# Kernel optimization log

Hardware: AMD Instinct MI355X
Metric: run time of the kernel (lower is better)

The kernel has to match this reference:

```python
import jax, jax.numpy as jnp
import numpy as np

# ---- static structure (from LastFMModel source) ----
COUNTS = (50000, 80000, 10000)   # user, item, tag node counts
FEAT, HID, INTRA, INTER = 256, 128, 64, 128
E = 500000                        # edges per metapath hop
# hops listed leaf->target as (src_type, dst_type, edge_type)
MP_USER = [[(0, 1, 0), (1, 0, 1)],
           [(0, 1, 0), (1, 2, 2), (2, 1, 3), (1, 0, 1)],
           [(0, 0, 4)]]
MP_ITEM = [[(1, 0, 1), (0, 1, 0)],
           [(1, 2, 2), (2, 1, 3)],
           [(1, 0, 1), (0, 0, 4), (0, 1, 0)]]
# get_gcn_encoder: etype in {1,2,4} -> encoder 1, {0,3} -> encoder 2
GCN_GROUP = {0: 2, 1: 1, 2: 1, 3: 2, 4: 1}
OFFSETS = (0, COUNTS[0], COUNTS[0] + COUNTS[1])


def _gen_edges(mps, rng):
    rows = []
    for hops in mps:
        for (st, dt, et) in hops:
            rows.append(np.stack([rng.integers(0, COUNTS[st], E),
                                  rng.integers(0, COUNTS[dt], E)]))
    return jnp.asarray(np.stack(rows), jnp.int32)


def setup_inputs() -> dict:
    rng = np.random.default_rng(0)
    ks = jax.random.split(jax.random.key(0), 16)
    n_total = sum(COUNTS)
    s = 0.05
    d = {}
    d['features'] = jax.random.normal(ks[0], (n_total, FEAT), jnp.float32)
    d['edges_user'] = _gen_edges(MP_USER, rng)
    d['edges_item'] = _gen_edges(MP_ITEM, rng)
    d['perm_user'] = jnp.asarray(rng.permutation(COUNTS[0]), jnp.int32)
    d['perm_item'] = jnp.asarray(rng.permutation(COUNTS[1]), jnp.int32)
    d['W_type'] = jax.random.normal(ks[1], (3, FEAT, HID), jnp.float32) * s
    d['b_type'] = jnp.zeros((3, HID), jnp.float32)
    d['comp_vec'] = jax.random.normal(ks[2], (5, HID), jnp.float32) * s
    d['W_gcn'] = jax.random.normal(ks[3], (3, HID, HID), jnp.float32) * s
    d['b_gcn'] = jnp.zeros((3, HID), jnp.float32)
    d['fc_u'] = jax.random.normal(ks[4], (3, HID, INTRA), jnp.float32) * s
    d['fcr_u'] = jax.random.normal(ks[5], (3, INTRA, HID), jnp.float32) * s
    d['V_u'] = jax.random.normal(ks[6], (3 * INTRA, INTER), jnp.float32) * s
    d['Vr_u'] = jax.random.normal(ks[7], (INTER, 3 * INTRA), jnp.float32) * s
    d['fc_i'] = jax.random.normal(ks[8], (3, HID, INTRA), jnp.float32) * s
    d['fcr_i'] = jax.random.normal(ks[9], (3, INTRA, HID), jnp.float32) * s
    d['V_i'] = jax.random.normal(ks[10], (3 * INTRA, INTER), jnp.float32) * s
    d['Vr_i'] = jax.random.normal(ks[11], (INTER, 3 * INTRA), jnp.float32) * s
    return d


def _propagate(h_src, src, dst, etype, n_dst, comp_vec, W_gcn, b_gcn):
    # CompGCN composition (elementwise) + GraphConv norm='right' (in-degree mean)
    msg = h_src[src] * comp_vec[etype]                                  # [E, HID]
    agg = jax.ops.segment_sum(msg, dst, num_segments=n_dst)
    deg = jax.ops.segment_sum(jnp.ones_like(dst, jnp.float32), dst, num_segments=n_dst)
    h = agg / jnp.clip(deg, 1.0)[:, None]
    g = GCN_GROUP[etype]
    return h @ W_gcn[g] + b_gcn[g]


def _fusion(outs, fc, fcr, V, Vr):
    # AutoMvFusion: per-view intra projection, shared inter fusion,
    # reconstruction loss + pairwise view orthogonality loss
    z_list = [jnp.tanh(h @ fc[p]) for p, h in enumerate(outs)]          # [N, INTRA] each
    z = jnp.concatenate(z_list, axis=1)                                 # [N, 3*INTRA]
    fused = z @ V                                                       # [N, INTER]
    z_rec = fused @ Vr
    re = jnp.float32(0.0)
    for p, h in enumerate(outs):
        h_rec = z_rec[:, p * INTRA:(p + 1) * INTRA] @ fcr[p]
        re = re + jnp.mean((h_rec - h) ** 2)
    orth = jnp.float32(0.0)
    for p in range(3):
        for q in range(p + 1, 3):
            g = z_list[p].T @ z_list[q]                                 # [INTRA, INTRA]
            orth = orth + jnp.mean(g ** 2)
    return fused, re + orth


def _run_layer(mp_hops, edges, perm, t_feats, comp_vec, W_gcn, b_gcn, fc, fcr, V, Vr):
    k = 0
    outs = []
    for hops in mp_hops:
        h = t_feats[hops[0][0]]           # leaf-type transformed features
        for (st, dt, et) in hops:
            h = _propagate(h, edges[k, 0], edges[k, 1], et, COUNTS[dt],
                           comp_vec, W_gcn, b_gcn)
            k += 1
        outs.append(h[perm])              # new_index_arrangement reindex
    return _fusion(outs, fc, fcr, V, Vr)


def reference(features, edges_user, edges_item, perm_user, perm_item,
              W_type, b_type, comp_vec, W_gcn, b_gcn,
              fc_u, fcr_u, V_u, Vr_u, fc_i, fcr_i, V_i, Vr_i):
    # NodeTransform: per-type linear + activation (dropout off at eval)
    t_feats = [jax.nn.relu(features[OFFSETS[t]:OFFSETS[t] + COUNTS[t]] @ W_type[t] + b_type[t])
               for t in range(3)]
    h_user, loss_u = _run_layer(MP_USER, edges_user, perm_user, t_feats,
                                comp_vec, W_gcn, b_gcn, fc_u, fcr_u, V_u, Vr_u)
    h_item, loss_i = _run_layer(MP_ITEM, edges_item, perm_item, t_feats,
                                comp_vec, W_gcn, b_gcn, fc_i, fcr_i, V_i, Vr_i)
    return h_user, h_item, loss_u + loss_i
```

## Files before the change

### kernel.cpp

```cpp
#include <hip/hip_runtime.h>

typedef unsigned short u16;
typedef unsigned int   u32;

#define ACT_NONE 0
#define ACT_RELU 1
#define ACT_TANH 2

#define E_EDGES 500000
#define RP_STRIDE 80004
#define NCH 62
#define CH 8192
#define HSTRIDE 19456

using s8vec = __attribute__((ext_vector_type(8))) short;
using f4vec = __attribute__((ext_vector_type(4))) float;

__device__ __forceinline__ float bf2f(u16 u) {
  union { u32 b; float f; } v; v.b = ((u32)u) << 16; return v.f;
}
__device__ __forceinline__ u16 f2bf(float x) {
  union { float f; u32 b; } v; v.f = x;
  u32 r = v.b + 0x7fffu + ((v.b >> 16) & 1u);
  return (u16)(r >> 16);
}
__device__ __forceinline__ void acc8(float* acc, uint4 v) {
  union { u32 b; float f; } cv;
  cv.b = v.x << 16;         acc[0] += cv.f;
  cv.b = v.x & 0xffff0000u; acc[1] += cv.f;
  cv.b = v.y << 16;         acc[2] += cv.f;
  cv.b = v.y & 0xffff0000u; acc[3] += cv.f;
  cv.b = v.z << 16;         acc[4] += cv.f;
  cv.b = v.z & 0xffff0000u; acc[5] += cv.f;
  cv.b = v.w << 16;         acc[6] += cv.f;
  cv.b = v.w & 0xffff0000u; acc[7] += cv.f;
}

struct TJob { const float* src; u16* dst; const float* scale; int R; int C; };
struct TBatch { TJob j[24]; };
__global__ __launch_bounds__(256) void transpose_b_k(TBatch b) {
  TJob jb = b.j[blockIdx.y];
  int i = blockIdx.x * 256 + threadIdx.x;
  if (i >= jb.R * jb.C) return;
  int r = i / jb.C, c = i % jb.C;
  float v = jb.src[i];
  if (jb.scale) v *= jb.scale[r];
  jb.dst[(size_t)c * jb.R + r] = f2bf(v);
}

struct IBatch { const int* perm[2]; int* ip[2]; int n[2]; };
__global__ __launch_bounds__(256) void iperm_b_k(IBatch b) {
  int y = blockIdx.y;
  int i = blockIdx.x * 256 + threadIdx.x;
  if (i < b.n[y]) b.ip[y][b.perm[y][i]] = i;
}

struct CsrP { int n[14]; int sh[14]; int P[14]; };

__global__ __launch_bounds__(256) void csr_hist_k(
    const int* __restrict__ eu, const int* __restrict__ ei,
    int* __restrict__ hista, CsrP cp) {
  const int hop = blockIdx.y, chunk = blockIdx.x;
  const int P = cp.P[hop], sh = cp.sh[hop];
  __shared__ int hist[320];
  for (int i = threadIdx.x; i < P; i += 256) hist[i] = 0;
  __syncthreads();
  const int* edges = (hop < 7) ? eu : ei;
  const int h7 = (hop < 7) ? hop : hop - 7;
  const int* dstp = edges + (size_t)(h7 * 2 + 1) * E_EDGES;
  const int e0 = chunk * CH;
  const int e1 = min(E_EDGES, e0 + CH);
  for (int e = e0 + threadIdx.x * 4; e < e1; e += 1024) {
    int4 d4 = *(const int4*)(dstp + e);
    atomicAdd(&hist[d4.x >> sh], 1);
    atomicAdd(&hist[d4.y >> sh], 1);
    atomicAdd(&hist[d4.z >> sh], 1);
    atomicAdd(&hist[d4.w >> sh], 1);
  }
  __syncthreads();
  for (int i = threadIdx.x; i < P; i += 256)
    hista[(size_t)hop * HSTRIDE + i * NCH + chunk] = hist[i];
}

__global__ __launch_bounds__(256) void csr_scan_k(int* __restrict__ hista, CsrP cp) {
  const int hop = blockIdx.x;
  const int L = cp.P[hop] * NCH;
  int* a = hista + (size_t)hop * HSTRIDE;
  const int per = (L + 255) >> 8;
  const int lo = threadIdx.x * per;
  const int hi = min(L, lo + per);
  int s = 0;
  for (int i = lo; i < hi; ++i) s += a[i];
  __shared__ int lds[256];
  lds[threadIdx.x] = s;
  __syncthreads();
  for (int off = 1; off < 256; off <<= 1) {
    int v = (threadIdx.x >= off) ? lds[threadIdx.x - off] : 0;
    __syncthreads();
    lds[threadIdx.x] += v;
    __syncthreads();
  }
  int run = threadIdx.x ? lds[threadIdx.x - 1] : 0;
  for (int i = lo; i < hi; ++i) { int v = a[i]; a[i] = run; run += v; }
}

__global__ __launch_bounds__(256) void csr_scatter_k(
    const int* __restrict__ eu, const int* __restrict__ ei,
    const int* __restrict__ hista, u32* __restrict__ bp, CsrP cp) {
  const int hop = blockIdx.y, chunk = blockIdx.x;
  const int P = cp.P[hop], sh = cp.sh[hop];
  const u32 fm = (1u << sh) - 1u;
  __shared__ int cur[320];
  for (int i = threadIdx.x; i < P; i += 256)
    cur[i] = hista[(size_t)hop * HSTRIDE + i * NCH + chunk];
  __syncthreads();
  const int* edges = (hop < 7) ? eu : ei;
  const int h7 = (hop < 7) ? hop : hop - 7;
  const int* srcp = edges + (size_t)(h7 * 2) * E_EDGES;
  const int* dstp = srcp + E_EDGES;
  u32* b = bp + (size_t)hop * E_EDGES;
  const int e0 = chunk * CH;
  const int e1 = min(E_EDGES, e0 + CH);
  for (int e = e0 + threadIdx.x * 4; e < e1; e += 1024) {
    int4 d4 = *(const int4*)(dstp + e);
    int4 s4 = *(const int4*)(srcp + e);
    int dd[4] = {d4.x, d4.y, d4.z, d4.w};
    int ss[4] = {s4.x, s4.y, s4.z, s4.w};
#pragma unroll
    for (int j = 0; j < 4; ++j) {
      int pos = atomicAdd(&cur[dd[j] >> sh], 1);
      b[pos] = (u32)ss[j] | (((u32)dd[j] & fm) << 24);
    }
  }
}

__global__ __launch_bounds__(256) void csr_fine_k(
    const u32* __restrict__ bp, const int* __restrict__ hista,
    int* __restrict__ rowptrb, int* __restrict__ esrcb, CsrP cp) {
  const int hop = blockIdx.y, p = blockIdx.x;
  const int P = cp.P[hop];
  if (p >= P) return;
  const int n = cp.n[hop], sh = cp.sh[hop], W = 1 << sh;
  const int* fl = hista + (size_t)hop * HSTRIDE;
  const int beg = fl[p * NCH];
  const int end = (p + 1 < P) ? fl[(p + 1) * NCH] : E_EDGES;
  const int nb = min(W, n - p * W);
  const int tid = threadIdx.x;

  __shared__ int fh[256];
  __shared__ int sc[256];
  __shared__ int cur[256];
  fh[tid] = 0;
  __syncthreads();
  const u32* b = bp + (size_t)hop * E_EDGES;
  for (int i = beg + tid; i < end; i += 256)
    atomicAdd(&fh[b[i] >> 24], 1);
  __syncthreads();
  sc[tid] = fh[tid];
  __syncthreads();
  for (int off = 1; off < 256; off <<= 1) {
    int v = (tid >= off) ? sc[tid - off] : 0;
    __syncthreads();
    sc[tid] += v;
    __syncthreads();
  }
  const int excl = tid ? sc[tid - 1] : 0;
  int* rowptr = rowptrb + (size_t)hop * RP_STRIDE;
  if (tid < nb) rowptr[p * W + tid] = beg + excl;
  cur[tid] = beg + excl;
  if (p == P - 1 && tid == 0) rowptr[n] = E_EDGES;
  __syncthreads();
  int* esrc = esrcb + (size_t)hop * E_EDGES;
  for (int i = beg + tid; i < end; i += 256) {
    u32 v = b[i];
    int pos = atomicAdd(&cur[v >> 24], 1);
    esrc[pos] = (int)(v & 0xFFFFFFu);
  }
}

struct HopJob {
  const u16* h; const int* rowptr; const int* esrc;
  const u16* Bt; const float* bias; u16* out;
  const int* iperm; int n; int permout;
};
struct HopBatch { HopJob j[6]; };

__global__ __launch_bounds__(256) void hop_b_k(HopBatch batch) {
  const HopJob jb = batch.j[blockIdx.y];
  const int rbase = blockIdx.x * 64;
  if (rbase >= jb.n) return;

  __shared__ u16 bts[128 * 128];
  const int tid = threadIdx.x;
  for (int i = tid; i < 128 * 16; i += 256) {
    int nn = i >> 4, g = i & 15;
    int gs = (g & 8) | ((g ^ nn) & 7);
    *(uint4*)(&bts[nn * 128 + gs * 8]) = *(const uint4*)(jb.Bt + (size_t)nn * 128 + g * 8);
  }
  __syncthreads();

  const int wave = tid >> 6;
  const int lane = tid & 63;
  const int kgrp = lane >> 4;
  const int lid  = lane & 15;
  const int d = rbase + wave * 16 + lid;

  float a0[8] = {0,0,0,0,0,0,0,0}, a1[8] = {0,0,0,0,0,0,0,0};
  float a2[8] = {0,0,0,0,0,0,0,0}, a3[8] = {0,0,0,0,0,0,0,0};
  int s0 = 0, s1 = 0;
  if (d < jb.n) { s0 = jb.rowptr[d]; s1 = jb.rowptr[d + 1]; }
  const u16* hk = jb.h + kgrp * 8;
  int i = s0;
  for (; i + 1 < s1; i += 2) {
    const u16* ra = hk + (size_t)jb.esrc[i] * 128;
    const u16* rb = hk + (size_t)jb.esrc[i + 1] * 128;
    uint4 va0 = *(const uint4*)(ra);      uint4 vb0 = *(const uint4*)(rb);
    uint4 va1 = *(const uint4*)(ra + 32); uint4 vb1 = *(const uint4*)(rb + 32);
    uint4 va2 = *(const uint4*)(ra + 64); uint4 vb2 = *(const uint4*)(rb + 64);
    uint4 va3 = *(const uint4*)(ra + 96); uint4 vb3 = *(const uint4*)(rb + 96);
    acc8(a0, va0); acc8(a1, va1); acc8(a2, va2); acc8(a3, va3);
    acc8(a0, vb0); acc8(a1, vb1); acc8(a2, vb2); acc8(a3, vb3);
  }
  if (i < s1) {
    const u16* ra = hk + (size_t)jb.esrc[i] * 128;
    acc8(a0, *(const uint4*)(ra));
    acc8(a1, *(const uint4*)(ra + 32));
    acc8(a2, *(const uint4*)(ra + 64));
    acc8(a3, *(const uint4*)(ra + 96));
  }
  const float rs = 1.0f / fmaxf((float)(s1 - s0), 1.0f);
  s8vec f0, f1, f2, f3;
#pragma unroll
  for (int j = 0; j < 8; ++j) f0[j] = (short)f2bf(a0[j] * rs);
#pragma unroll
  for (int j = 0; j < 8; ++j) f1[j] = (short)f2bf(a1[j] * rs);
#pragma unroll
  for (int j = 0; j < 8; ++j) f2[j] = (short)f2bf(a2[j] * rs);
#pragma unroll
  for (int j = 0; j < 8; ++j) f3[j] = (short)f2bf(a3[j] * rs);

#pragma unroll
  for (int t = 0; t < 8; ++t) {
    f4vec c = {0.f, 0.f, 0.f, 0.f};
    const int bn = t * 16 + lid;
    int g = kgrp;
    int gs = (g & 8) | ((g ^ bn) & 7);
    c = __builtin_amdgcn_mfma_f32_16x16x32_bf16(f0, *(const s8vec*)(&bts[bn * 128 + gs * 8]), c, 0, 0, 0);
    g = 4 + kgrp; gs = (g & 8) | ((g ^ bn) & 7);
    c = __builtin_amdgcn_mfma_f32_16x16x32_bf16(f1, *(const s8vec*)(&bts[bn * 128 + gs * 8]), c, 0, 0, 0);
    g = 8 + kgrp; gs = (g & 8) | ((g ^ bn) & 7);
    c = __builtin_amdgcn_mfma_f32_16x16x32_bf16(f2, *(const s8vec*)(&bts[bn * 128 + gs * 8]), c, 0, 0, 0);
    g = 12 + kgrp; gs = (g & 8) | ((g ^ bn) & 7);
    c = __builtin_amdgcn_mfma_f32_16x16x32_bf16(f3, *(const s8vec*)(&bts[bn * 128 + gs * 8]), c, 0, 0, 0);
    const int col = bn;
    const float bb = jb.bias[col];
#pragma unroll
    for (int j = 0; j < 4; ++j) {
      int r = rbase + wave * 16 + kgrp * 4 + j;
      if (r < jb.n) {
        float v = c[j] + bb;
        int ro = jb.permout ? jb.iperm[r] : r;
        jb.out[(size_t)ro * 128 + col] = f2bf(v);
      }
    }
  }
}

struct GemmJob {
  const void* A; const u16* Bt; const float* bias; void* C;
  const u16* target; float* loss; u16* Ct; int M;
};
struct GemmBatch { GemmJob j[3]; };

template <int K, int N, int ACT, int AMODE, bool CF32, bool SQDIFF, bool CTR>
__global__ __launch_bounds__(256) void gemm_b_k(
    GemmBatch batch, int ldA, int ldC, int ldCt) {
  static_assert(K % 32 == 0 && N % 16 == 0, "");
  const GemmJob jb = batch.j[blockIdx.y];
  const int rbase0 = blockIdx.x * 64;
  if (rbase0 >= jb.M) return;

  __shared__ u16 bts[N * K];
  __shared__ float red[4];

  const int tid = threadIdx.x;
  for (int i = tid; i < N * (K / 8); i += 256) {
    int n = i / (K / 8);
    int g = i % (K / 8);
    int gs = (g & ~7) | ((g ^ n) & 7);
    *(uint4*)(&bts[n * K + gs * 8]) = *(const uint4*)(jb.Bt + (size_t)n * K + g * 8);
  }
  __syncthreads();

  const int wave = tid >> 6;
  const int lane = tid & 63;
  const int kgrp = lane >> 4;
  const int rbase = rbase0 + wave * 16;
  const int rowA = rbase + (lane & 15);
  const bool av = rowA < jb.M;

  s8vec afr[K / 32];
  if constexpr (AMODE == 1) {
    const float* arow = (const float*)jb.A + (size_t)rowA * ldA;
#pragma unroll
    for (int kt = 0; kt < K / 32; ++kt) {
      s8vec fr = {0, 0, 0, 0, 0, 0, 0, 0};
      if (av) {
        const float* p = arow + kt * 32 + kgrp * 8;
        float4 fa = *(const float4*)(p);
        float4 fb = *(const float4*)(p + 4);
        fr[0] = (short)f2bf(fa.x); fr[1] = (short)f2bf(fa.y);
        fr[2] = (short)f2bf(fa.z); fr[3] = (short)f2bf(fa.w);
        fr[4] = (short)f2bf(fb.x); fr[5] = (short)f2bf(fb.y);
        fr[6] = (short)f2bf(fb.z); fr[7] = (short)f2bf(fb.w);
      }
      afr[kt] = fr;
    }
  } else {
    const u16* arow = (const u16*)jb.A + (size_t)rowA * ldA;
#pragma unroll
    for (int kt = 0; kt < K / 32; ++kt) {
      s8vec fr = {0, 0, 0, 0, 0, 0, 0, 0};
      if (av) fr = *(const s8vec*)(arow + kt * 32 + kgrp * 8);
      afr[kt] = fr;
    }
  }

  float sqsum = 0.0f;
#pragma unroll
  for (int t = 0; t < N / 16; ++t) {
    f4vec acc = {0.f, 0.f, 0.f, 0.f};
    const int bn = t * 16 + (lane & 15);
#pragma unroll
    for (int kt = 0; kt < K / 32; ++kt) {
      int g = kt * 4 + kgrp;
      int gs = (g & ~7) | ((g ^ bn) & 7);
      s8vec bfr = *(const s8vec*)(&bts[bn * K + gs * 8]);
      acc = __builtin_amdgcn_mfma_f32_16x16x32_bf16(afr[kt], bfr, acc, 0, 0, 0);
    }
    const int col = t * 16 + (lane & 15);
    float bb = jb.bias ? jb.bias[col] : 0.0f;
#pragma unroll
    for (int j = 0; j < 4; ++j) {
      int r = rbase + kgrp * 4 + j;
      if (r < jb.M) {
        float v = acc[j] + bb;
        if constexpr (ACT == ACT_RELU) v = fmaxf(v, 0.0f);
        if constexpr (ACT == ACT_TANH) v = tanhf(v);
        if constexpr (SQDIFF) {
          float dd = v - bf2f(jb.target[(size_t)r * N + col]);
          sqsum += dd * dd;
        } else if constexpr (CF32) {
          ((float*)jb.C)[(size_t)r * ldC + col] = v;
        } else {
          ((u16*)jb.C)[(size_t)r * ldC + col] = f2bf(v);
        }
        if constexpr (CTR) {
          jb.Ct[(size_t)col * ldCt + r] = f2bf(v);
        }
      }
    }
  }

  if constexpr (SQDIFF) {
#pragma unroll
    for (int off = 32; off > 0; off >>= 1) sqsum += __shfl_down(sqsum, off);
    if (lane == 0) red[wave] = sqsum;
    __syncthreads();
    if (tid == 0) atomicAdd(jb.loss, red[0] + red[1] + red[2] + red[3]);
  }
}

#define GRAM_NKB 40
__global__ __launch_bounds__(256) void gram_k(
    const u16* __restrict__ zt, int NP, float* __restrict__ G3) {
  const int pair = blockIdx.y;
  const int p = (pair == 2) ? 1 : 0;
  const int q = (pair == 0) ? 1 : 2;
  const int wave = threadIdx.x >> 6;
  const int lane = threadIdx.x & 63;
  const int kgrp = lane >> 4, lid = lane & 15;

  const int KC = (((NP + GRAM_NKB - 1) / GRAM_NKB) + 31) & ~31;
  const int kbeg = blockIdx.x * KC;
  const int kend = min(NP, kbeg + KC);

  const u16* arow = zt + (size_t)(p * 64 + wave * 16 + lid) * NP;
  const u16* brow0 = zt + (size_t)(q * 64 + 0 * 16 + lid) * NP;
  const u16* brow1 = zt + (size_t)(q * 64 + 1 * 16 + lid) * NP;
  const u16* brow2 = zt + (size_t)(q * 64 + 2 * 16 + lid) * NP;
  const u16* brow3 = zt + (size_t)(q * 64 + 3 * 16 + lid) * NP;

  f4vec acc0 = {0.f, 0.f, 0.f, 0.f};
  f4vec acc1 = {0.f, 0.f, 0.f, 0.f};
  f4vec acc2 = {0.f, 0.f, 0.f, 0.f};
  f4vec acc3 = {0.f, 0.f, 0.f, 0.f};

  for (int k0 = kbeg; k0 < kend; k0 += 32) {
    const int ko = k0 + kgrp * 8;
    s8vec af = *(const s8vec*)(arow + ko);
    s8vec b0 = *(const s8vec*)(brow0 + ko);
    s8vec b1 = *(const s8vec*)(brow1 + ko);
    s8vec b2 = *(const s8vec*)(brow2 + ko);
    s8vec b3 = *(const s8vec*)(brow3 + ko);
    acc0 = __builtin_amdgcn_mfma_f32_16x16x32_bf16(af, b0, acc0, 0, 0, 0);
    acc1 = __builtin_amdgcn_mfma_f32_16x16x32_bf16(af, b1, acc1, 0, 0, 0);
    acc2 = __builtin_amdgcn_mfma_f32_16x16x32_bf16(af, b2, acc2, 0, 0, 0);
    acc3 = __builtin_amdgcn_mfma_f32_16x16x32_bf16(af, b3, acc3, 0, 0, 0);
  }

  float* g = G3 + (size_t)pair * 4096;
  const int mrow = wave * 16 + kgrp * 4;
#pragma unroll
  for (int j = 0; j < 4; ++j) {
    atomicAdd(&g[(mrow + j) * 64 + 0 * 16 + lid], acc0[j]);
    atomicAdd(&g[(mrow + j) * 64 + 1 * 16 + lid], acc1[j]);
    atomicAdd(&g[(mrow + j) * 64 + 2 * 16 + lid], acc2[j]);
    atomicAdd(&g[(mrow + j) * 64 + 3 * 16 + lid], acc3[j]);
  }
}

__global__ __launch_bounds__(256) void loss_k(
    const float* __restrict__ G, const float* __restrict__ RE,
    float* __restrict__ out) {
  float s = 0.f;
  for (int i = threadIdx.x; i < 2 * 3 * 4096; i += 256) { float g = G[i]; s += g * g; }
#pragma unroll
  for (int off = 32; off > 0; off >>= 1) s += __shfl_down(s, off);
  __shared__ float red[4];
  int wave = threadIdx.x >> 6, lane = threadIdx.x & 63;
  if (lane == 0) red[wave] = s;
  __syncthreads();
  if (threadIdx.x == 0) {
    float orth = (red[0] + red[1] + red[2] + red[3]) / 4096.0f;
    float loss = orth + RE[0] / (50000.0f * 128.0f) + RE[1] / (80000.0f * 128.0f);
    out[0] = loss;
  }
}

static const int COUNTS_H[3] = {50000, 80000, 10000};
static const int OFFS_H[3]   = {0, 50000, 130000};
static const int GRP_H[5]    = {2, 1, 1, 2, 1};
static const int HOPN[14] = {80000, 50000, 80000, 10000, 80000, 50000, 50000,
                             50000, 80000, 10000, 80000, 50000, 50000, 80000};

extern "C" void kernel_launch(void* const* d_in, const int* in_sizes, int n_in,
                              void* d_out, int out_size, void* d_ws, size_t ws_size,
                              hipStream_t stream) {
  (void)in_sizes; (void)n_in; (void)out_size; (void)ws_size;

  const float* features = (const float*)d_in[0];
  const int* e_user   = (const int*)d_in[1];
  const int* e_item   = (const int*)d_in[2];
  const int* perm_u   = (const int*)d_in[3];
  const int* perm_i   = (const int*)d_in[4];
  const float* W_type = (const float*)d_in[5];
  const float* b_type = (const float*)d_in[6];
  const float* comp   = (const float*)d_in[7];
  const float* W_gcn  = (const float*)d_in[8];
  const float* b_gcn  = (const float*)d_in[9];
  const float* fc[2]  = {(const float*)d_in[10], (const float*)d_in[14]};
  const float* fcr[2] = {(const float*)d_in[11], (const float*)d_in[15]};
  const float* V[2]   = {(const float*)d_in[12], (const float*)d_in[16]};
  const float* Vr[2]  = {(const float*)d_in[13], (const float*)d_in[17]};
  float* out = (float*)d_out;

  char* base = (char*)d_ws;
  size_t off = 0;
  auto alloc = [&](size_t b) -> void* {
    void* p = base + off;
    off = (off + b + 255) & ~(size_t)255;
    return p;
  };
  u16* TF    = (u16*)alloc(140000ull * 128 * 2);
  u16* HB    = (u16*)alloc(330000ull * 128 * 2);
  u16* OUTSu = (u16*)alloc(3ull * 50000 * 128 * 2);
  u16* OUTSi = (u16*)alloc(3ull * 80000 * 128 * 2);
  int* HISTA    = (int*)alloc(14ull * HSTRIDE * 4);
  int* ROWPTR14 = (int*)alloc(14ull * RP_STRIDE * 4);
  int* ESRC14   = (int*)alloc(14ull * E_EDGES * 4);
  int* IPERM    = (int*)alloc(130000ull * 4);
  u16* WT_TYPE = (u16*)alloc(3ull * 128 * 256 * 2);
  u16* BT_HOP  = (u16*)alloc(5ull * 128 * 128 * 2);
  u16* FCT     = (u16*)alloc(6ull * 64 * 128 * 2);
  u16* VT      = (u16*)alloc(2ull * 128 * 192 * 2);
  u16* VRT     = (u16*)alloc(2ull * 192 * 128 * 2);
  u16* FCRT    = (u16*)alloc(6ull * 128 * 64 * 2);
  float* G   = (float*)alloc((2 * 3 * 4096 + 2) * 4);
  float* RE  = G + 2 * 3 * 4096;

  u32* BP   = (u32*)HB;
  u16* Z    = HB;
  u16* ZREC = HB + 80000ull * 192;
  u16* ZT   = (u16*)HISTA;

  const int hbrow[7] = {0, 80000, 160000, 170000, 220000, 230000, 280000};
  auto HBp = [&](int c) { return HB + (size_t)hbrow[c] * 128; };
  auto RP  = [&](int g) { return ROWPTR14 + (size_t)g * RP_STRIDE; };
  auto ES  = [&](int g) { return ESRC14 + (size_t)g * E_EDGES; };
  auto BT  = [&](int et) { return BT_HOP + (size_t)et * 128 * 128; };
  auto BG  = [&](int et) { return b_gcn + (size_t)GRP_H[et] * 128; };

  TBatch tb;
  int tj = 0;
  for (int t = 0; t < 3; ++t)
    tb.j[tj++] = {W_type + (size_t)t * 256 * 128, WT_TYPE + (size_t)t * 128 * 256, nullptr, 256, 128};
  for (int et = 0; et < 5; ++et)
    tb.j[tj++] = {W_gcn + (size_t)GRP_H[et] * 128 * 128, BT_HOP + (size_t)et * 128 * 128,
                  comp + (size_t)et * 128, 128, 128};
  for (int L = 0; L < 2; ++L)
    for (int p = 0; p < 3; ++p)
      tb.j[tj++] = {fc[L] + (size_t)p * 128 * 64, FCT + (size_t)(L * 3 + p) * 64 * 128, nullptr, 128, 64};
  for (int L = 0; L < 2; ++L)
    for (int p = 0; p < 3; ++p)
      tb.j[tj++] = {fcr[L] + (size_t)p * 64 * 128, FCRT + (size_t)(L * 3 + p) * 128 * 64, nullptr, 64, 128};
  for (int L = 0; L < 2; ++L)
    tb.j[tj++] = {V[L], VT + (size_t)L * 128 * 192, nullptr, 192, 128};
  for (int L = 0; L < 2; ++L)
    tb.j[tj++] = {Vr[L], VRT + (size_t)L * 192 * 128, nullptr, 128, 192};
  transpose_b_k<<<dim3(128, 24), 256, 0, stream>>>(tb);

  IBatch ib;
  ib.perm[0] = perm_u; ib.ip[0] = IPERM;          ib.n[0] = 50000;
  ib.perm[1] = perm_i; ib.ip[1] = IPERM + 50000;  ib.n[1] = 80000;
  iperm_b_k<<<dim3(313, 2), 256, 0, stream>>>(ib);

  CsrP cpp;
  for (int g = 0; g < 14; ++g) {
    cpp.n[g] = HOPN[g];
    cpp.sh[g] = (HOPN[g] <= 10000) ? 6 : 8;
    cpp.P[g] = (HOPN[g] + (1 << cpp.sh[g]) - 1) >> cpp.sh[g];
  }
  csr_hist_k<<<dim3(NCH, 14), 256, 0, stream>>>(e_user, e_item, HISTA, cpp);
  csr_scan_k<<<dim3(14), 256, 0, stream>>>(HISTA, cpp);
  csr_scatter_k<<<dim3(NCH, 14), 256, 0, stream>>>(e_user, e_item, HISTA, BP, cpp);
  csr_fine_k<<<dim3(313, 14), 256, 0, stream>>>(BP, HISTA, ROWPTR14, ESRC14, cpp);
  hipMemsetAsync(G, 0, (2 * 3 * 4096 + 2) * 4, stream);

  {
    GemmBatch nb;
    for (int t = 0; t < 3; ++t)
      nb.j[t] = {features + (size_t)OFFS_H[t] * 256, WT_TYPE + (size_t)t * 128 * 256,
                 b_type + (size_t)t * 128, TF + (size_t)OFFS_H[t] * 128,
                 nullptr, nullptr, nullptr, COUNTS_H[t]};
    gemm_b_k<256, 128, ACT_RELU, 1, false, false, false>
        <<<dim3(1250, 3), 256, 0, stream>>>(nb, 256, 128, 0);
  }

  const u16* TF0 = TF;
  const u16* TF1 = TF + 50000ull * 128;
  const int* IPu = IPERM;
  const int* IPi = IPERM + 50000;

  HopBatch L0, L1, L2, L3;
  L0.j[0] = {TF0, RP(0),  ES(0),  BT(0), BG(0), HBp(0), nullptr, 80000, 0};
  L0.j[1] = {TF0, RP(2),  ES(2),  BT(0), BG(0), HBp(1), nullptr, 80000, 0};
  L0.j[2] = {TF0, RP(6),  ES(6),  BT(4), BG(4), OUTSu + 2ull * 50000 * 128, IPu, 50000, 1};
  L0.j[3] = {TF1, RP(7),  ES(7),  BT(1), BG(1), HBp(3), nullptr, 50000, 0};
  L0.j[4] = {TF1, RP(9),  ES(9),  BT(2), BG(2), HBp(4), nullptr, 10000, 0};
  L0.j[5] = {TF1, RP(11), ES(11), BT(1), BG(1), HBp(5), nullptr, 50000, 0};
  L1.j[0] = {HBp(0), RP(1),  ES(1),  BT(1), BG(1), OUTSu, IPu, 50000, 1};
  L1.j[1] = {HBp(1), RP(3),  ES(3),  BT(2), BG(2), HBp(2), nullptr, 10000, 0};
  L1.j[2] = {HBp(3), RP(8),  ES(8),  BT(0), BG(0), OUTSi, IPi, 80000, 1};
  L1.j[3] = {HBp(4), RP(10), ES(10), BT(3), BG(3), OUTSi + 1ull * 80000 * 128, IPi, 80000, 1};
  L1.j[4] = {HBp(5), RP(12), ES(12), BT(4), BG(4), HBp(6), nullptr, 50000, 0};
  L1.j[5] = L1.j[4];
  L2.j[0] = {HBp(2), RP(4),  ES(4),  BT(3), BG(3), HBp(0), nullptr, 80000, 0};
  L2.j[1] = {HBp(6), RP(13), ES(13), BT(0), BG(0), OUTSi + 2ull * 80000 * 128, IPi, 80000, 1};
  L2.j[2] = L2.j[1]; L2.j[3] = L2.j[1]; L2.j[4] = L2.j[1]; L2.j[5] = L2.j[1];
  L3.j[0] = {HBp(0), RP(5), ES(5), BT(1), BG(1), OUTSu + 1ull * 50000 * 128, IPu, 50000, 1};
  L3.j[1] = L3.j[0]; L3.j[2] = L3.j[0]; L3.j[3] = L3.j[0]; L3.j[4] = L3.j[0]; L3.j[5] = L3.j[0];

  hop_b_k<<<dim3(1250, 6), 256, 0, stream>>>(L0);
  hop_b_k<<<dim3(1250, 5), 256, 0, stream>>>(L1);
  hop_b_k<<<dim3(1250, 2), 256, 0, stream>>>(L2);
  hop_b_k<<<dim3(782, 1), 256, 0, stream>>>(L3);

  for (int L = 0; L < 2; ++L) {
    const int nL = L ? 80000 : 50000;
    const int NP = (nL + 31) & ~31;
    u16* OUTS_L = L ? OUTSi : OUTSu;
    const size_t pstride = (size_t)nL * 128;
    const dim3 gg((unsigned)((nL + 63) / 64));

    if (NP != nL)
      hipMemsetAsync(ZT, 0, (size_t)192 * NP * 2, stream);

    GemmBatch fb;
    for (int p = 0; p < 3; ++p)
      fb.j[p] = {OUTS_L + p * pstride, FCT + (size_t)(L * 3 + p) * 64 * 128, nullptr,
                 Z + p * 64, nullptr, nullptr, ZT + (size_t)p * 64 * NP, nL};
    gemm_b_k<128, 64, ACT_TANH, 0, false, false, true>
        <<<dim3(gg.x, 3), 256, 0, stream>>>(fb, 128, 192, NP);

    gram_k<<<dim3(GRAM_NKB, 3), 256, 0, stream>>>(ZT, NP, G + (size_t)L * 3 * 4096);

    float* fused = out + (L ? 6400000 : 0);
    GemmBatch vb;
    vb.j[0] = {Z, VT + (size_t)L * 128 * 192, nullptr, fused, nullptr, nullptr, nullptr, nL};
    vb.j[1] = vb.j[0]; vb.j[2] = vb.j[0];
    gemm_b_k<192, 128, ACT_NONE, 0, true, false, false>
        <<<dim3(gg.x, 1), 256, 0, stream>>>(vb, 192, 128, 0);

    GemmBatch rb;
    rb.j[0] = {fused, VRT + (size_t)L * 192 * 128, nullptr, ZREC, nullptr, nullptr, nullptr, nL};
    rb.j[1] = rb.j[0]; rb.j[2] = rb.j[0];
    gemm_b_k<128, 192, ACT_NONE, 1, false, false, false>
        <<<dim3(gg.x, 1), 256, 0, stream>>>(rb, 128, 192, 0);

    GemmBatch sb;
    for (int p = 0; p < 3; ++p)
      sb.j[p] = {ZREC + p * 64, FCRT + (size_t)(L * 3 + p) * 128 * 64, nullptr,
                 nullptr, OUTS_L + p * pstride, RE + L, nullptr, nL};
    gemm_b_k<64, 128, ACT_NONE, 0, false, true, false>
        <<<dim3(gg.x, 3), 256, 0, stream>>>(sb, 192, 0, 0);
  }

  loss_k<<<1, 256, 0, stream>>>(G, RE, out + 16640000);
}
```

Before: 1.109 ms.

## Fuse fusion-stage V, Vr and reconstruction-loss GEMMs into one kernel, batch both layers

Three GEMM launches per layer (V projection, Vr reconstruction, per-path fcr reconstruction with squared-difference loss) become one vfuse_k kernel. It keeps the fused tile and reconstructed Z in shared memory instead of writing ZREC to global and reading it back. The user and item layers are also batched into single launches for the tanh GEMM and the Gram kernel, giving separate Z/ZT buffers per layer. B operands in the fused kernel are read straight from global memory rather than staged in LDS, which may add load traffic in exchange for less intermediate round-tripping.

```diff
diff --git a/kernel.cpp b/kernel.cpp
--- a/kernel.cpp
+++ b/kernel.cpp
@@ -239,6 +239,13 @@
 #pragma unroll
   for (int j = 0; j < 8; ++j) f3[j] = (short)f2bf(a3[j] * rs);
 
+  int rout[4];
+#pragma unroll
+  for (int j = 0; j < 4; ++j) {
+    int rv = rbase + wave * 16 + kgrp * 4 + j;
+    rout[j] = (rv < jb.n) ? (jb.permout ? jb.iperm[rv] : rv) : -1;
+  }
+
 #pragma unroll
   for (int t = 0; t < 8; ++t) {
     f4vec c = {0.f, 0.f, 0.f, 0.f};
@@ -252,15 +259,12 @@
     c = __builtin_amdgcn_mfma_f32_16x16x32_bf16(f2, *(const s8vec*)(&bts[bn * 128 + gs * 8]), c, 0, 0, 0);
     g = 12 + kgrp; gs = (g & 8) | ((g ^ bn) & 7);
     c = __builtin_amdgcn_mfma_f32_16x16x32_bf16(f3, *(const s8vec*)(&bts[bn * 128 + gs * 8]), c, 0, 0, 0);
-    const int col = bn;
-    const float bb = jb.bias[col];
+    const float bb = jb.bias[bn];
 #pragma unroll
     for (int j = 0; j < 4; ++j) {
-      int r = rbase + wave * 16 + kgrp * 4 + j;
-      if (r < jb.n) {
+      if (rout[j] >= 0) {
         float v = c[j] + bb;
-        int ro = jb.permout ? jb.iperm[r] : r;
-        jb.out[(size_t)ro * 128 + col] = f2bf(v);
+        jb.out[(size_t)rout[j] * 128 + bn] = f2bf(v);
       }
     }
   }
@@ -268,20 +272,19 @@
 
 struct GemmJob {
   const void* A; const u16* Bt; const float* bias; void* C;
-  const u16* target; float* loss; u16* Ct; int M;
+  u16* Ct; int M; int ldCt;
 };
-struct GemmBatch { GemmJob j[3]; };
-
-template <int K, int N, int ACT, int AMODE, bool CF32, bool SQDIFF, bool CTR>
+struct GemmBatch { GemmJob j[6]; };
+
+template <int K, int N, int ACT, int AMODE, bool CF32, bool CTR>
 __global__ __launch_bounds__(256) void gemm_b_k(
-    GemmBatch batch, int ldA, int ldC, int ldCt) {
+    GemmBatch batch, int ldA, int ldC) {
   static_assert(K % 32 == 0 && N % 16 == 0, "");
   const GemmJob jb = batch.j[blockIdx.y];
   const int rbase0 = blockIdx.x * 64;
   if (rbase0 >= jb.M) return;
 
   __shared__ u16 bts[N * K];
-  __shared__ float red[4];
 
   const int tid = threadIdx.x;
   for (int i = tid; i < N * (K / 8); i += 256) {
@@ -326,7 +329,6 @@
     }
   }
 
-  float sqsum = 0.0f;
 #pragma unroll
   for (int t = 0; t < N / 16; ++t) {
     f4vec acc = {0.f, 0.f, 0.f, 0.f};
@@ -347,34 +349,150 @@
         float v = acc[j] + bb;
         if constexpr (ACT == ACT_RELU) v = fmaxf(v, 0.0f);
         if constexpr (ACT == ACT_TANH) v = tanhf(v);
-        if constexpr (SQDIFF) {
-          float dd = v - bf2f(jb.target[(size_t)r * N + col]);
-          sqsum += dd * dd;
-        } else if constexpr (CF32) {
+        if constexpr (CF32) {
           ((float*)jb.C)[(size_t)r * ldC + col] = v;
         } else {
           ((u16*)jb.C)[(size_t)r * ldC + col] = f2bf(v);
         }
         if constexpr (CTR) {
-          jb.Ct[(size_t)col * ldCt + r] = f2bf(v);
+          jb.Ct[(size_t)col * jb.ldCt + r] = f2bf(v);
         }
       }
     }
   }
-
-  if constexpr (SQDIFF) {
-#pragma unroll
-    for (int off = 32; off > 0; off >>= 1) sqsum += __shfl_down(sqsum, off);
-    if (lane == 0) red[wave] = sqsum;
-    __syncthreads();
-    if (tid == 0) atomicAdd(jb.loss, red[0] + red[1] + red[2] + red[3]);
-  }
+}
+
+struct VFJob {
+  const u16* Z;
+  const u16* VT;
+  const u16* VRT;
+  const u16* FCRT;
+  const u16* target;
+  float* fused;
+  float* loss;
+  int M;
+};
+
+__global__ __launch_bounds__(256) void vfuse_k(VFJob j0, VFJob j1) {
+  const VFJob jb = blockIdx.y ? j1 : j0;
+  const int rbase = blockIdx.x * 64;
+  if (rbase >= jb.M) return;
+
+  __shared__ u16 ftile[64 * 128];
+  __shared__ u16 ztile[64 * 192];
+  __shared__ float red[4];
+
+  const int tid = threadIdx.x;
+  const int wave = tid >> 6;
+  const int lane = tid & 63;
+  const int kgrp = lane >> 4;
+  const int lid  = lane & 15;
+  const int arow_l = wave * 16 + lid;
+  const int rowA = rbase + arow_l;
+  const bool av = rowA < jb.M;
+
+  s8vec az[6];
+#pragma unroll
+  for (int kt = 0; kt < 6; ++kt) {
+    s8vec fr = {0, 0, 0, 0, 0, 0, 0, 0};
+    if (av) fr = *(const s8vec*)(jb.Z + (size_t)rowA * 192 + kt * 32 + kgrp * 8);
+    az[kt] = fr;
+  }
+#pragma unroll
+  for (int t = 0; t < 8; ++t) {
+    f4vec acc = {0.f, 0.f, 0.f, 0.f};
+    const int bn = t * 16 + lid;
+    const u16* brow = jb.VT + (size_t)bn * 192;
+#pragma unroll
+    for (int kt = 0; kt < 6; ++kt)
+      acc = __builtin_amdgcn_mfma_f32_16x16x32_bf16(az[kt], *(const s8vec*)(brow + kt * 32 + kgrp * 8), acc, 0, 0, 0);
+    const int g = bn >> 3;
+#pragma unroll
+    for (int j = 0; j < 4; ++j) {
+      int rl = wave * 16 + kgrp * 4 + j;
+      int r = rbase + rl;
+      float v = acc[j];
+      int gs = (g & 8) | ((g ^ rl) & 7);
+      if (r < jb.M) {
+        jb.fused[(size_t)r * 128 + bn] = v;
+        ftile[rl * 128 + gs * 8 + (bn & 7)] = f2bf(v);
+      } else {
+        ftile[rl * 128 + gs * 8 + (bn & 7)] = 0;
+      }
+    }
+  }
+  __syncthreads();
+
+  s8vec af[4];
+#pragma unroll
+  for (int kt = 0; kt < 4; ++kt) {
+    int ga = kt * 4 + kgrp;
+    int gs = (ga & 8) | ((ga ^ arow_l) & 7);
+    af[kt] = *(const s8vec*)(&ftile[arow_l * 128 + gs * 8]);
+  }
+#pragma unroll
+  for (int t = 0; t < 12; ++t) {
+    f4vec acc = {0.f, 0.f, 0.f, 0.f};
+    const int bn = t * 16 + lid;
+    const u16* brow = jb.VRT + (size_t)bn * 128;
+#pragma unroll
+    for (int kt = 0; kt < 4; ++kt)
+      acc = __builtin_amdgcn_mfma_f32_16x16x32_bf16(af[kt], *(const s8vec*)(brow + kt * 32 + kgrp * 8), acc, 0, 0, 0);
+    const int g = bn >> 3;
+#pragma unroll
+    for (int j = 0; j < 4; ++j) {
+      int rl = wave * 16 + kgrp * 4 + j;
+      int gs = (g & ~7) | ((g ^ rl) & 7);
+      ztile[rl * 192 + gs * 8 + (bn & 7)] = f2bf(acc[j]);
+    }
+  }
+  __syncthreads();
+
+  float sqsum = 0.0f;
+#pragma unroll
+  for (int p = 0; p < 3; ++p) {
+    s8vec aq[2];
+#pragma unroll
+    for (int kt = 0; kt < 2; ++kt) {
+      int ga = p * 8 + kt * 4 + kgrp;
+      int gs = (ga & ~7) | ((ga ^ arow_l) & 7);
+      aq[kt] = *(const s8vec*)(&ztile[arow_l * 192 + gs * 8]);
+    }
+    const u16* fp = jb.FCRT + (size_t)p * 128 * 64;
+    const u16* tgt = jb.target + (size_t)p * jb.M * 128;
+#pragma unroll
+    for (int t = 0; t < 8; ++t) {
+      f4vec acc = {0.f, 0.f, 0.f, 0.f};
+      const int bn = t * 16 + lid;
+      const u16* brow = fp + (size_t)bn * 64;
+#pragma unroll
+      for (int kt = 0; kt < 2; ++kt)
+        acc = __builtin_amdgcn_mfma_f32_16x16x32_bf16(aq[kt], *(const s8vec*)(brow + kt * 32 + kgrp * 8), acc, 0, 0, 0);
+#pragma unroll
+      for (int j = 0; j < 4; ++j) {
+        int r = rbase + wave * 16 + kgrp * 4 + j;
+        if (r < jb.M) {
+          float dd = acc[j] - bf2f(tgt[(size_t)r * 128 + bn]);
+          sqsum += dd * dd;
+        }
+      }
+    }
+  }
+#pragma unroll
+  for (int off = 32; off > 0; off >>= 1) sqsum += __shfl_down(sqsum, off);
+  if (lane == 0) red[wave] = sqsum;
+  __syncthreads();
+  if (tid == 0) atomicAdd(jb.loss, red[0] + red[1] + red[2] + red[3]);
 }
 
 #define GRAM_NKB 40
 __global__ __launch_bounds__(256) void gram_k(
-    const u16* __restrict__ zt, int NP, float* __restrict__ G3) {
-  const int pair = blockIdx.y;
+    const u16* __restrict__ zt0, const u16* __restrict__ zt1,
+    int NP0, int NP1, float* __restrict__ G) {
+  const int layer = blockIdx.y / 3;
+  const int pair = blockIdx.y % 3;
+  const u16* zt = layer ? zt1 : zt0;
+  const int NP = layer ? NP1 : NP0;
   const int p = (pair == 2) ? 1 : 0;
   const int q = (pair == 0) ? 1 : 2;
   const int wave = threadIdx.x >> 6;
@@ -409,7 +527,7 @@
     acc3 = __builtin_amdgcn_mfma_f32_16x16x32_bf16(af, b3, acc3, 0, 0, 0);
   }
 
-  float* g = G3 + (size_t)pair * 4096;
+  float* g = G + (size_t)layer * 3 * 4096 + (size_t)pair * 4096;
   const int mrow = wave * 16 + kgrp * 4;
 #pragma unroll
   for (int j = 0; j < 4; ++j) {
@@ -490,9 +608,11 @@
   float* RE  = G + 2 * 3 * 4096;
 
   u32* BP   = (u32*)HB;
-  u16* Z    = HB;
-  u16* ZREC = HB + 80000ull * 192;
-  u16* ZT   = (u16*)HISTA;
+  u16* Z0   = HB;
+  u16* Z1   = HB + 9600000ull;
+  const int NP0 = 50016, NP1 = 80032;
+  u16* ZT0  = (u16*)HISTA;
+  u16* ZT1  = TF;
 
   const int hbrow[7] = {0, 80000, 160000, 170000, 220000, 230000, 280000};
   auto HBp = [&](int c) { return HB + (size_t)hbrow[c] * 128; };
@@ -538,13 +658,13 @@
   hipMemsetAsync(G, 0, (2 * 3 * 4096 + 2) * 4, stream);
 
   {
-    GemmBatch nb;
+    GemmBatch nb = {};
     for (int t = 0; t < 3; ++t)
       nb.j[t] = {features + (size_t)OFFS_H[t] * 256, WT_TYPE + (size_t)t * 128 * 256,
                  b_type + (size_t)t * 128, TF + (size_t)OFFS_H[t] * 128,
-                 nullptr, nullptr, nullptr, COUNTS_H[t]};
-    gemm_b_k<256, 128, ACT_RELU, 1, false, false, false>
-        <<<dim3(1250, 3), 256, 0, stream>>>(nb, 256, 128, 0);
+                 nullptr, COUNTS_H[t], 0};
+    gemm_b_k<256, 128, ACT_RELU, 1, false, false>
+        <<<dim3(1250, 3), 256, 0, stream>>>(nb, 256, 128);
   }
 
   const u16* TF0 = TF;
@@ -576,44 +696,28 @@
   hop_b_k<<<dim3(1250, 2), 256, 0, stream>>>(L2);
   hop_b_k<<<dim3(782, 1), 256, 0, stream>>>(L3);
 
-  for (int L = 0; L < 2; ++L) {
-    const int nL = L ? 80000 : 50000;
-    const int NP = (nL + 31) & ~31;
-    u16* OUTS_L = L ? OUTSi : OUTSu;
-    const size_t pstride = (size_t)nL * 128;
-    const dim3 gg((unsigned)((nL + 63) / 64));
-
-    if (NP != nL)
-      hipMemsetAsync(ZT, 0, (size_t)192 * NP * 2, stream);
-
-    GemmBatch fb;
-    for (int p = 0; p < 3; ++p)
-      fb.j[p] = {OUTS_L + p * pstride, FCT + (size_t)(L * 3 + p) * 64 * 128, nullptr,
-                 Z + p * 64, nullptr, nullptr, ZT + (size_t)p * 64 * NP, nL};
-    gemm_b_k<128, 64, ACT_TANH, 0, false, false, true>
-        <<<dim3(gg.x, 3), 256, 0, stream>>>(fb, 128, 192, NP);
-
-    gram_k<<<dim3(GRAM_NKB, 3), 256, 0, stream>>>(ZT, NP, G + (size_t)L * 3 * 4096);
-
-    float* fused = out + (L ? 6400000 : 0);
-    GemmBatch vb;
-    vb.j[0] = {Z, VT + (size_t)L * 128 * 192, nullptr, fused, nullptr, nullptr, nullptr, nL};
-    vb.j[1] = vb.j[0]; vb.j[2] = vb.j[0];
-    gemm_b_k<192, 128, ACT_NONE, 0, true, false, false>
-        <<<dim3(gg.x, 1), 256, 0, stream>>>(vb, 192, 128, 0);
-
-    GemmBatch rb;
-    rb.j[0] = {fused, VRT + (size_t)L * 192 * 128, nullptr, ZREC, nullptr, nullptr, nullptr, nL};
-    rb.j[1] = rb.j[0]; rb.j[2] = rb.j[0];
-    gemm_b_k<128, 192, ACT_NONE, 1, false, false, false>
-        <<<dim3(gg.x, 1), 256, 0, stream>>>(rb, 128, 192, 0);
-
-    GemmBatch sb;
-    for (int p = 0; p < 3; ++p)
-      sb.j[p] = {ZREC + p * 64, FCRT + (size_t)(L * 3 + p) * 128 * 64, nullptr,
-                 nullptr, OUTS_L + p * pstride, RE + L, nullptr, nL};
-    gemm_b_k<64, 128, ACT_NONE, 0, false, true, false>
-        <<<dim3(gg.x, 3), 256, 0, stream>>>(sb, 192, 0, 0);
+  hipMemsetAsync(ZT0, 0, (size_t)192 * NP0 * 2, stream);
+  hipMemsetAsync(ZT1, 0, (size_t)192 * NP1 * 2, stream);
+
+  {
+    GemmBatch fb = {};
+    for (int p = 0; p < 3; ++p) {
+      fb.j[p]     = {OUTSu + (size_t)p * 50000 * 128, FCT + (size_t)p * 64 * 128, nullptr,
+                     Z0 + p * 64, ZT0 + (size_t)p * 64 * NP0, 50000, NP0};
+      fb.j[p + 3] = {OUTSi + (size_t)p * 80000 * 128, FCT + (size_t)(3 + p) * 64 * 128, nullptr,
+                     Z1 + p * 64, ZT1 + (size_t)p * 64 * NP1, 80000, NP1};
+    }
+    gemm_b_k<128, 64, ACT_TANH, 0, false, true>
+        <<<dim3(1250, 6), 256, 0, stream>>>(fb, 128, 192);
+  }
+
+  gram_k<<<dim3(GRAM_NKB, 6), 256, 0, stream>>>(ZT0, ZT1, NP0, NP1, G);
+
+  {
+    VFJob j0 = {Z0, VT, VRT, FCRT, OUTSu, out, RE + 0, 50000};
+    VFJob j1 = {Z1, VT + (size_t)128 * 192, VRT + (size_t)192 * 128, FCRT + (size_t)3 * 128 * 64,
+                OUTSi, out + 6400000, RE + 1, 80000};
+    vfuse_k<<<dim3(1250, 2), 256, 0, stream>>>(j0, j1);
   }
 
   loss_k<<<1, 256, 0, stream>>>(G, RE, out + 16640000);
```

Result: faster. 1.043 ms (-6.0%).
